# Optimization experiments

Measured on AMD Instinct MI355X. Metric: run time of the kernel, lower is better.

Reference implementation:

```python
import jax, jax.numpy as jnp
import numpy as np

L, B, S, D = 8, 1, 4096, 2048
H, KVH, HD = 16, 2, 128
Q = 32
THETA = 1e6
MROPE = (16, 24, 24)  # mrope_section, sums to HD//2
EPS = 1e-6


def setup_inputs() -> dict:
    key = jax.random.key(0)
    ks = jax.random.split(key, 8)
    hidden_states = jax.random.normal(ks[0], (L, B, S, D), dtype=jnp.float32)
    ln_w = jax.random.uniform(ks[1], (L, D), dtype=jnp.float32, minval=0.5, maxval=1.5)
    q_w = jax.random.normal(ks[2], (L, D, H * HD), dtype=jnp.float32) * 0.02
    q_b = jax.random.normal(ks[3], (L, H * HD), dtype=jnp.float32) * 0.02
    k_w = jax.random.normal(ks[4], (L, D, KVH * HD), dtype=jnp.float32) * 0.02
    k_b = jax.random.normal(ks[5], (L, KVH * HD), dtype=jnp.float32) * 0.02
    position_ids = jax.random.randint(ks[6], (3, B, S), 0, S, dtype=jnp.int32)
    q_idx = jnp.sort(jax.random.randint(ks[7], (Q,), 0, S, dtype=jnp.int32))
    return {"hidden_states": hidden_states, "ln_w": ln_w, "q_w": q_w, "q_b": q_b,
            "k_w": k_w, "k_b": k_b, "position_ids": position_ids, "q_idx": q_idx}


def _rot_half(x):
    h = x.shape[-1] // 2
    return jnp.concatenate([-x[..., h:], x[..., :h]], axis=-1)


def _mrope_combine(t):
    # t: (3, B, S, HD). Split last dim per 2*mrope_section, chunk i taken from axis i%3.
    parts, off = [], 0
    for i, sec in enumerate(MROPE):
        w = 2 * sec
        parts.append(t[i % 3, :, :, off:off + w])
        off += w
    return jnp.concatenate(parts, axis=-1)[:, None, :, :]  # (B, 1, S, HD)


def reference(hidden_states, ln_w, q_w, q_b, k_w, k_b, position_ids, q_idx):
    # Rotary embeddings from 3D mRoPE position ids
    inv_freq = 1.0 / (THETA ** (jnp.arange(0, HD, 2, dtype=jnp.float32) / HD))  # (HD/2,)
    freqs = position_ids.astype(jnp.float32)[..., None] * inv_freq  # (3, B, S, HD/2)
    emb = jnp.concatenate([freqs, freqs], axis=-1)  # (3, B, S, HD)
    cos = _mrope_combine(jnp.cos(emb))  # (B, 1, S, HD)
    sin = _mrope_combine(jnp.sin(emb))
    cos_q = cos[:, :, q_idx, :]  # (B, 1, Q, HD)
    sin_q = sin[:, :, q_idx, :]
    # Eager causal mask sliced at query rows: (Q, S)
    mask_add = jnp.where(jnp.arange(S)[None, :] > q_idx[:, None], -1e9, 0.0).astype(jnp.float32)

    scale = 1.0 / np.sqrt(HD).astype(np.float32)

    def per_layer(hs, lw, qw, qb, kw, kb):
        # RMSNorm (input_layernorm)
        var = jnp.mean(jnp.square(hs), axis=-1, keepdims=True)
        x = hs * jax.lax.rsqrt(var + EPS) * lw  # (B, S, D)
        xq = x[:, q_idx, :]  # (B, Q, D)
        k = (jnp.einsum('bsd,de->bse', x, kw) + kb).reshape(B, S, KVH, HD).transpose(0, 2, 1, 3)
        q = (jnp.einsum('bqd,de->bqe', xq, qw) + qb).reshape(B, Q, H, HD).transpose(0, 2, 1, 3)
        k = jnp.repeat(k, H // KVH, axis=1)  # repeat_kv -> (B, H, S, HD)
        k = k * cos + _rot_half(k) * sin
        q = q * cos_q + _rot_half(q) * sin_q
        scores = jnp.einsum('bhqd,bhkd->bhqk', q, k) * scale  # (B, H, Q, S)
        scores = scores + mask_add[None, None]
        return jax.nn.softmax(scores.astype(jnp.float32), axis=-1)

    return jax.vmap(per_layer)(hidden_states, ln_w, q_w, q_b, k_w, k_b)  # (L, B, H, Q, S)
```

## Files before the change

### kernel.cpp

```cpp
#include <hip/hip_runtime.h>
#include <hip/hip_bf16.h>
#include <math.h>

#define LYR 8
#define SEQ 4096
#define DIM 2048
#define NH 16
#define HD 128
#define NQ 32
#define NKV 256
#define NQE 2048

typedef __attribute__((ext_vector_type(8))) short short8;
typedef __attribute__((ext_vector_type(4))) float f32x4;

#define WS_IRQ   0
#define WS_ABLOB 256
#define WS_COS   524544
#define WS_SIN   1048832
#define WS_QBUF  1573120
#define WS_PART  2097408
#define WS_W2    4194560
#define WS_KBLOB 8388864
#define WS_QBLOB 16777472

__device__ __forceinline__ short f2bf(float x) {
  __hip_bfloat16 h = __float2bfloat16(x);
  return *(short*)&h;
}
__device__ __forceinline__ float bf2f(short s) {
  unsigned u = ((unsigned)(unsigned short)s) << 16;
  return __uint_as_float(u);
}

#define GLOAD16(srcp, dstp) \
  __builtin_amdgcn_global_load_lds( \
      (const __attribute__((address_space(1))) unsigned int*)(srcp), \
      (__attribute__((address_space(3))) unsigned int*)(dstp), 16, 0, 0)

#define RBAR() asm volatile("s_waitcnt lgkmcnt(0)\n\ts_barrier" ::: "memory")

__global__ __launch_bounds__(256) void prep_kernel(
    const float* __restrict__ ln_w, const float* __restrict__ k_w,
    short* __restrict__ W2) {
  int kb = blockIdx.x, l = blockIdx.y, t = threadIdx.x;
  const float* kwl = k_w + (size_t)l * DIM * NKV;
  const float* lnl = ln_w + l * DIM;
  short* blob = W2 + (size_t)(l * 64 + kb) * 16384;
  #pragma unroll
  for (int i = 0; i < 4; ++i) {
    int p = t + i * 256;
    int fi = p >> 6, lane = p & 63;
    int n = fi * 16 + (lane & 15);
    int k0 = kb * 32 + (lane >> 4) * 8;
    short hi8[8], lo8[8];
    #pragma unroll
    for (int e = 0; e < 8; ++e) {
      float v = lnl[k0 + e] * kwl[(size_t)(k0 + e) * NKV + n];
      short h = f2bf(v);
      hi8[e] = h;
      lo8[e] = f2bf(v - bf2f(h));
    }
    *(short8*)(blob + p * 8) = *(short8*)hi8;
    *(short8*)(blob + 8192 + p * 8) = *(short8*)lo8;
  }
}

__global__ __launch_bounds__(256) void rmsq_kernel(const float* __restrict__ hs,
                                                   const int* __restrict__ q_idx,
                                                   float* __restrict__ irq) {
  int qi = blockIdx.x, l = blockIdx.y, t = threadIdx.x;
  int s = q_idx[qi];
  const float* row = hs + ((size_t)l * SEQ + s) * DIM;
  float4 v0 = *(const float4*)(row + t * 4);
  float4 v1 = *(const float4*)(row + t * 4 + 1024);
  float acc = v0.x*v0.x + v0.y*v0.y + v0.z*v0.z + v0.w*v0.w
            + v1.x*v1.x + v1.y*v1.y + v1.z*v1.z + v1.w*v1.w;
  #pragma unroll
  for (int off = 32; off >= 1; off >>= 1) acc += __shfl_down(acc, off);
  __shared__ float red[4];
  if ((t & 63) == 0) red[t >> 6] = acc;
  __syncthreads();
  if (t == 0) {
    float tot = red[0] + red[1] + red[2] + red[3];
    irq[l * NQ + qi] = rsqrtf(tot / (float)DIM + 1e-6f);
  }
}

__global__ void cossin_kernel(const int* __restrict__ pos_ids,
                              float* __restrict__ cost, float* __restrict__ sint) {
  int idx = blockIdx.x * 256 + threadIdx.x;
  int s = idx >> 7, d = idx & 127;
  int t = (d < 32) ? 0 : (d < 80 ? 1 : 2);
  int j = d & 63;
  double invf = pow(1000000.0, -(double)j / 64.0);
  double ph = (double)pos_ids[t * SEQ + s] * invf;
  cost[idx] = (float)cos(ph);
  sint[idx] = (float)sin(ph);
}

__global__ __launch_bounds__(256) void xqt_kernel(
    const float* __restrict__ hs, const float* __restrict__ ln_w,
    const int* __restrict__ q_idx, const float* __restrict__ irq,
    short* __restrict__ Ablob) {
  __shared__ int qix[32];
  __shared__ float qir[32];
  int l = blockIdx.x, t = threadIdx.x;
  if (t < 32) { qix[t] = q_idx[t]; qir[t] = irq[l * NQ + t]; }
  __syncthreads();
  int lane = t & 63, g4 = t >> 6;
  short* base = Ablob + (size_t)l * 131072;
  int row = lane & 15, kgl = lane >> 4;
  for (int i = 0; i < 64; ++i) {
    int group = g4 * 64 + i;
    int kb = group >> 2, half = (group >> 1) & 1, mf = group & 1;
    int r = row + mf * 16;
    int k0 = kb * 32 + kgl * 8;
    const float* src = hs + ((size_t)l * SEQ + qix[r]) * DIM + k0;
    const float* lnp = ln_w + l * DIM + k0;
    float ir = qir[r];
    float4 v0 = *(const float4*)src;
    float4 v1 = *(const float4*)(src + 4);
    float4 w0 = *(const float4*)lnp;
    float4 w1 = *(const float4*)(lnp + 4);
    float av[8] = {v0.x*w0.x, v0.y*w0.y, v0.z*w0.z, v0.w*w0.w,
                   v1.x*w1.x, v1.y*w1.y, v1.z*w1.z, v1.w*w1.w};
    short o8[8];
    #pragma unroll
    for (int e = 0; e < 8; ++e) {
      float v = av[e] * ir;
      short h = f2bf(v);
      o8[e] = half ? f2bf(v - bf2f(h)) : h;
    }
    *(short8*)(base + group * 512 + lane * 8) = *(short8*)o8;
  }
}

__global__ __launch_bounds__(256) void kgemm_kernel(
    const float* __restrict__ hs, const short* __restrict__ W2,
    const float* __restrict__ k_b, const float* __restrict__ cost,
    const float* __restrict__ sint, short* __restrict__ Kblob) {
  __shared__ __align__(1024) char SM[67072];

  int t = threadIdx.x;
  int fid = blockIdx.x;
  int l = fid & 7, sb = fid >> 3;
  int s0 = sb * 64;
  int lane = t & 63, w = t >> 6;
  int fr = lane & 15, kg = lane >> 4;
  int arow = t >> 2, akg = t & 3;

  const float* hrow = hs + ((size_t)l * SEQ + s0 + arow) * DIM + akg * 8;
  const char* wbase = (const char*)(W2 + (size_t)l * 64 * 16384);
  const char* wfrag = wbase + w * 1024 + lane * 16;

  int amf = arow >> 4;
  int awoff = amf * 1024 + (((akg * 16 + (arow & 15)) * 16) ^ (akg << 5));
  int aroff = (lane * 16) ^ ((lane >> 4) << 5);

  f32x4 acc[4][4];
  #pragma unroll
  for (int mf = 0; mf < 4; ++mf)
    #pragma unroll
    for (int nf = 0; nf < 4; ++nf) acc[mf][nf] = (f32x4){0.f, 0.f, 0.f, 0.f};
  float sq = 0.f;
  float4 rA0, rA1, rB0, rB1;
  short8 B0h[4], B0l[4], B1h[4], B1l[4];

  {
    #pragma unroll
    for (int nf = 0; nf < 4; ++nf) {
      B0h[nf] = *(const short8*)(wfrag + nf * 4096);
      B0l[nf] = *(const short8*)(wfrag + nf * 4096 + 16384);
    }
    float4 a0 = *(const float4*)(hrow);
    float4 a1 = *(const float4*)(hrow + 4);
    float av[8] = {a0.x, a0.y, a0.z, a0.w, a1.x, a1.y, a1.z, a1.w};
    short hi8[8], lo8[8];
    #pragma unroll
    for (int e = 0; e < 8; ++e) {
      sq += av[e] * av[e];
      short h = f2bf(av[e]);
      hi8[e] = h;
      lo8[e] = f2bf(av[e] - bf2f(h));
    }
    *(short8*)(SM + awoff) = *(short8*)hi8;
    *(short8*)(SM + 4096 + awoff) = *(short8*)lo8;
    rA0 = *(const float4*)(hrow + 32);
    rA1 = *(const float4*)(hrow + 36);
  }
  RBAR();

#define KSTEP(KB, CA0, CA1, NA0, NA1, UBH, UBL, PBH, PBL) do { \
    int buf_ = (KB) & 1; \
    char* asb_ = SM + buf_ * 8192; \
    if ((KB) < 63) { \
      const char* bsrc_ = wfrag + (size_t)((KB) + 1) * 32768; \
      _Pragma("unroll") \
      for (int nf = 0; nf < 4; ++nf) { \
        PBH[nf] = *(const short8*)(bsrc_ + nf * 4096); \
        PBL[nf] = *(const short8*)(bsrc_ + nf * 4096 + 16384); \
      } \
    } \
    if ((KB) < 62) { \
      NA0 = *(const float4*)(hrow + ((KB) + 2) * 32); \
      NA1 = *(const float4*)(hrow + ((KB) + 2) * 32 + 4); \
    } \
    short8 ah_[4], al_[4]; \
    _Pragma("unroll") \
    for (int mf = 0; mf < 4; ++mf) { \
      ah_[mf] = *(const short8*)(asb_ + mf * 1024 + aroff); \
      al_[mf] = *(const short8*)(asb_ + 4096 + mf * 1024 + aroff); \
    } \
    __builtin_amdgcn_s_setprio(1); \
    _Pragma("unroll") \
    for (int nf = 0; nf < 4; ++nf) { \
      _Pragma("unroll") \
      for (int mf = 0; mf < 4; ++mf) { \
        acc[mf][nf] = __builtin_amdgcn_mfma_f32_16x16x32_bf16(ah_[mf], UBH[nf], acc[mf][nf], 0, 0, 0); \
        acc[mf][nf] = __builtin_amdgcn_mfma_f32_16x16x32_bf16(ah_[mf], UBL[nf], acc[mf][nf], 0, 0, 0); \
        acc[mf][nf] = __builtin_amdgcn_mfma_f32_16x16x32_bf16(al_[mf], UBH[nf], acc[mf][nf], 0, 0, 0); \
      } \
    } \
    __builtin_amdgcn_s_setprio(0); \
    if ((KB) < 63) { \
      char* asn_ = SM + (buf_ ^ 1) * 8192; \
      float av_[8] = {CA0.x, CA0.y, CA0.z, CA0.w, CA1.x, CA1.y, CA1.z, CA1.w}; \
      short hi8_[8], lo8_[8]; \
      _Pragma("unroll") \
      for (int e = 0; e < 8; ++e) { \
        sq += av_[e] * av_[e]; \
        short h_ = f2bf(av_[e]); \
        hi8_[e] = h_; \
        lo8_[e] = f2bf(av_[e] - bf2f(h_)); \
      } \
      *(short8*)(asn_ + awoff) = *(short8*)hi8_; \
      *(short8*)(asn_ + 4096 + awoff) = *(short8*)lo8_; \
    } \
    RBAR(); \
  } while (0)

  for (int kb2 = 0; kb2 < 32; ++kb2) {
    KSTEP(2 * kb2,     rA0, rA1, rB0, rB1, B0h, B0l, B1h, B1l);
    KSTEP(2 * kb2 + 1, rB0, rB1, rA0, rA1, B1h, B1l, B0h, B0l);
  }
#undef KSTEP

  sq += __shfl_xor(sq, 1);
  sq += __shfl_xor(sq, 2);
  float* irs = (float*)(SM + 66560);
  if ((t & 3) == 0) irs[arow] = rsqrtf(sq / (float)DIM + 1e-6f);
  __syncthreads();

  float* Kraw = (float*)SM;
  int j = w * 16 + fr;
  float bias0 = k_b[l * NKV + j];
  float bias1 = k_b[l * NKV + j + 64];
  float bias2 = k_b[l * NKV + j + 128];
  float bias3 = k_b[l * NKV + j + 192];
  #pragma unroll
  for (int mf = 0; mf < 4; ++mf) {
    #pragma unroll
    for (int r = 0; r < 4; ++r) {
      int row = mf * 16 + kg * 4 + r;
      int s = s0 + row;
      float ir = irs[row];
      float v0 = acc[mf][0][r] * ir + bias0;
      float v1 = acc[mf][1][r] * ir + bias1;
      float v2 = acc[mf][2][r] * ir + bias2;
      float v3 = acc[mf][3][r] * ir + bias3;
      float cj = cost[s * HD + j], sj = sint[s * HD + j];
      float cj2 = cost[s * HD + j + 64], sj2 = sint[s * HD + j + 64];
      float* kr = Kraw + row * 260;
      kr[j]       = v0 * cj - v1 * sj;
      kr[j + 64]  = v1 * cj2 + v0 * sj2;
      kr[j + 128] = v2 * cj - v3 * sj;
      kr[j + 192] = v3 * cj2 + v2 * sj2;
    }
  }
  __syncthreads();

  int kc = sb >> 1, fb = (sb & 1) * 4;
  #pragma unroll
  for (int i = 0; i < 8; ++i) {
    int c = t + i * 256;
    int lc = c & 63, fl = (c >> 6) & 3, ts = (c >> 8) & 3, kv = c >> 10;
    int key = fl * 16 + (lc & 15);
    int d0 = kv * 128 + ts * 32 + (lc >> 4) * 8;
    float4 x0 = *(const float4*)(Kraw + key * 260 + d0);
    float4 x1 = *(const float4*)(Kraw + key * 260 + d0 + 4);
    float av[8] = {x0.x, x0.y, x0.z, x0.w, x1.x, x1.y, x1.z, x1.w};
    short hi8[8], lo8[8];
    #pragma unroll
    for (int e = 0; e < 8; ++e) {
      short h = f2bf(av[e]);
      hi8[e] = h;
      lo8[e] = f2bf(av[e] - bf2f(h));
    }
    short* bb = Kblob + (size_t)((l * 2 + kv) * 32 + kc) * 32768
              + (size_t)((ts * 2 + 0) * 8 + fb + fl) * 512 + lc * 8;
    *(short8*)bb = *(short8*)hi8;
    *(short8*)(bb + 4096) = *(short8*)lo8;
  }
}

__global__ __launch_bounds__(512) void qgemm_kernel(
    const float* __restrict__ q_w, const short* __restrict__ Ablob,
    float* __restrict__ part) {
  __shared__ __align__(1024) char SM[131072];
  int t = threadIdx.x;
  int nc = blockIdx.x, ks = blockIdx.y, l = blockIdx.z;
  int lane = t & 63, w = t >> 6;
  int fr = lane & 15, kg = lane >> 4;
  const char* abase = (const char*)(Ablob + (size_t)l * 131072 + (size_t)ks * 32768);
  const float* qwl = q_w + (size_t)l * DIM * NQE;

  #pragma unroll
  for (int c = 0; c < 8; ++c) {
    int chunk = w * 8 + c;
    GLOAD16(abase + chunk * 1024 + lane * 16, SM + chunk * 1024);
  }
  #pragma unroll
  for (int c = 0; c < 4; ++c) {
    int r = w * 4 + c;
    GLOAD16((const char*)(qwl + (size_t)(ks * 512 + r) * NQE + nc * 256) + lane * 16,
            SM + 65536 + r * 1024 + lane * 16);
  }
  f32x4 acc[2][2];
  #pragma unroll
  for (int mf = 0; mf < 2; ++mf)
    #pragma unroll
    for (int nf = 0; nf < 2; ++nf) acc[mf][nf] = (f32x4){0.f, 0.f, 0.f, 0.f};
  __syncthreads();

  for (int ts = 0; ts < 16; ++ts) {
    int buf = ts & 1;
    if (ts < 15) {
      #pragma unroll
      for (int c = 0; c < 4; ++c) {
        int r = w * 4 + c;
        GLOAD16((const char*)(qwl + (size_t)(ks * 512 + (ts + 1) * 32 + r) * NQE + nc * 256) + lane * 16,
                SM + 65536 + (buf ^ 1) * 32768 + r * 1024 + lane * 16);
      }
    }
    short8 ah[2], al[2];
    #pragma unroll
    for (int mf = 0; mf < 2; ++mf) {
      ah[mf] = *(const short8*)(SM + ts * 4096 + mf * 1024 + lane * 16);
      al[mf] = *(const short8*)(SM + ts * 4096 + 2048 + mf * 1024 + lane * 16);
    }
    const float* bt = (const float*)(SM + 65536 + buf * 32768);
    #pragma unroll
    for (int nf = 0; nf < 2; ++nf) {
      int c = w * 32 + nf * 16 + fr;
      short bh8[8], bl8[8];
      #pragma unroll
      for (int e = 0; e < 8; ++e) {
        float v = bt[(kg * 8 + e) * 256 + c];
        short h = f2bf(v);
        bh8[e] = h;
        bl8[e] = f2bf(v - bf2f(h));
      }
      short8 bh = *(short8*)bh8, bl = *(short8*)bl8;
      #pragma unroll
      for (int mf = 0; mf < 2; ++mf) {
        acc[mf][nf] = __builtin_amdgcn_mfma_f32_16x16x32_bf16(ah[mf], bh, acc[mf][nf], 0, 0, 0);
        acc[mf][nf] = __builtin_amdgcn_mfma_f32_16x16x32_bf16(ah[mf], bl, acc[mf][nf], 0, 0, 0);
        acc[mf][nf] = __builtin_amdgcn_mfma_f32_16x16x32_bf16(al[mf], bh, acc[mf][nf], 0, 0, 0);
      }
    }
    __syncthreads();
  }

  #pragma unroll
  for (int mf = 0; mf < 2; ++mf) {
    #pragma unroll
    for (int r = 0; r < 4; ++r) {
      int row = mf * 16 + kg * 4 + r;
      float* prow = part + ((size_t)((ks * LYR + l) * NQ + row)) * NQE + nc * 256;
      #pragma unroll
      for (int nf = 0; nf < 2; ++nf) {
        int col = w * 32 + nf * 16 + fr;
        prow[col] = acc[mf][nf][r];
      }
    }
  }
}

__global__ __launch_bounds__(256) void qred_kernel(
    const float* __restrict__ part, const float* __restrict__ q_b,
    float* __restrict__ Qbuf) {
  int idx = blockIdx.x * 256 + threadIdx.x;
  int n = idx & 2047, q = (idx >> 11) & 31, l = idx >> 16;
  float v = q_b[l * NQE + n];
  #pragma unroll
  for (int ks = 0; ks < 4; ++ks)
    v += part[((size_t)((ks * LYR + l) * NQ + q)) * NQE + n];
  Qbuf[((size_t)l * NQ + q) * NQE + n] = v;
}

__global__ __launch_bounds__(256) void qpack_kernel(
    const float* __restrict__ Qbuf, const float* __restrict__ cost,
    const float* __restrict__ sint, const int* __restrict__ q_idx,
    short* __restrict__ Qblob) {
  int kv = blockIdx.x, l = blockIdx.y, t = threadIdx.x;
  short* blob = Qblob + (size_t)(l * 2 + kv) * 65536;
  #pragma unroll
  for (int i = 0; i < 16; ++i) {
    int p = t + i * 256;
    int ts = p >> 10, f = (p >> 6) & 15, lane = p & 63;
    int row = f * 16 + (lane & 15);
    int hh = row >> 5, q = row & 31;
    int h = kv * 8 + hh;
    int d0 = ts * 32 + (lane >> 4) * 8;
    int s = q_idx[q];
    const float* qrow = Qbuf + ((size_t)l * NQ + q) * NQE + h * HD;
    const float* ct = cost + s * HD;
    const float* st = sint + s * HD;
    short hi8[8], lo8[8];
    #pragma unroll
    for (int e = 0; e < 8; ++e) {
      int d = d0 + e;
      float x = qrow[d];
      float xp = qrow[d ^ 64];
      float v = (d < 64) ? (x * ct[d] - xp * st[d]) : (x * ct[d] + xp * st[d]);
      short h2 = f2bf(v);
      hi8[e] = h2;
      lo8[e] = f2bf(v - bf2f(h2));
    }
    *(short8*)(blob + ((ts * 2 + 0) * 16 + f) * 512 + lane * 8) = *(short8*)hi8;
    *(short8*)(blob + ((ts * 2 + 1) * 16 + f) * 512 + lane * 8) = *(short8*)lo8;
  }
}

__global__ __launch_bounds__(512) void scores_kernel(
    const short* __restrict__ Qblob, const short* __restrict__ Kblob,
    const int* __restrict__ q_idx, float* __restrict__ out) {
  __shared__ short Qs[2][16384];
  __shared__ short Ks[2][8192];
  __shared__ int qiv[32];
  int t = threadIdx.x;
  int kc = blockIdx.x, kv = blockIdx.y, l = blockIdx.z;
  int lane = t & 63, w = t >> 6;
  int wm = w >> 1, wn = w & 1;
  if (t < 32) qiv[t] = q_idx[t];
  const char* qsrc = (const char*)(Qblob + (size_t)(l * 2 + kv) * 65536);
  const char* ksrc = (const char*)(Kblob + (size_t)((l * 2 + kv) * 32 + kc) * 32768);
  #pragma unroll
  for (int c = 0; c < 4; ++c) {
    int off = (w * 4 + c) * 1024;
    GLOAD16(qsrc + off + lane * 16, (char*)Qs[0] + off);
  }
  #pragma unroll
  for (int c = 0; c < 2; ++c) {
    int off = (w * 2 + c) * 1024;
    GLOAD16(ksrc + off + lane * 16, (char*)Ks[0] + off);
  }
  f32x4 acc[4][4];
  #pragma unroll
  for (int mf = 0; mf < 4; ++mf)
    #pragma unroll
    for (int nf = 0; nf < 4; ++nf) acc[mf][nf] = (f32x4){0.f, 0.f, 0.f, 0.f};
  __syncthreads();
  for (int ts = 0; ts < 4; ++ts) {
    int buf = ts & 1;
    if (ts < 3) {
      const char* qs = qsrc + (ts + 1) * 32768;
      const char* ks = ksrc + (ts + 1) * 16384;
      #pragma unroll
      for (int c = 0; c < 4; ++c) {
        int off = (w * 4 + c) * 1024;
        GLOAD16(qs + off + lane * 16, (char*)Qs[(ts + 1) & 1] + off);
      }
      #pragma unroll
      for (int c = 0; c < 2; ++c) {
        int off = (w * 2 + c) * 1024;
        GLOAD16(ks + off + lane * 16, (char*)Ks[(ts + 1) & 1] + off);
      }
    }
    short8 ah[4], al[4];
    #pragma unroll
    for (int mf = 0; mf < 4; ++mf) {
      int f = wm * 4 + mf;
      ah[mf] = *(const short8*)(Qs[buf] + f * 512 + lane * 8);
      al[mf] = *(const short8*)(Qs[buf] + 8192 + f * 512 + lane * 8);
    }
    #pragma unroll
    for (int nf = 0; nf < 4; ++nf) {
      int f = wn * 4 + nf;
      short8 bh = *(const short8*)(Ks[buf] + f * 512 + lane * 8);
      short8 bl = *(const short8*)(Ks[buf] + 4096 + f * 512 + lane * 8);
      #pragma unroll
      for (int mf = 0; mf < 4; ++mf) {
        acc[mf][nf] = __builtin_amdgcn_mfma_f32_16x16x32_bf16(ah[mf], bh, acc[mf][nf], 0, 0, 0);
        acc[mf][nf] = __builtin_amdgcn_mfma_f32_16x16x32_bf16(ah[mf], bl, acc[mf][nf], 0, 0, 0);
        acc[mf][nf] = __builtin_amdgcn_mfma_f32_16x16x32_bf16(al[mf], bh, acc[mf][nf], 0, 0, 0);
      }
    }
    __syncthreads();
  }
  const float scale = 0.088388347648318447f;
  #pragma unroll
  for (int mf = 0; mf < 4; ++mf) {
    #pragma unroll
    for (int r = 0; r < 4; ++r) {
      int rr = wm * 64 + mf * 16 + (lane >> 4) * 4 + r;
      int hh = rr >> 5, q = rr & 31;
      int qv = qiv[q];
      float* orow = out + (((size_t)(l * NH + kv * 8 + hh)) * NQ + q) * SEQ;
      #pragma unroll
      for (int nf = 0; nf < 4; ++nf) {
        int key = kc * 128 + (wn * 4 + nf) * 16 + (lane & 15);
        orow[key] = (key > qv) ? -1e9f : acc[mf][nf][r] * scale;
      }
    }
  }
}

__global__ __launch_bounds__(256) void softmax_kernel(float* __restrict__ out) {
  size_t row = blockIdx.x;
  float* p = out + row * SEQ;
  int t = threadIdx.x;
  float4 v[4];
  float mx = -1e30f;
  #pragma unroll
  for (int i = 0; i < 4; ++i) {
    v[i] = *(const float4*)(p + t * 4 + i * 1024);
    mx = fmaxf(mx, fmaxf(fmaxf(v[i].x, v[i].y), fmaxf(v[i].z, v[i].w)));
  }
  #pragma unroll
  for (int off = 32; off >= 1; off >>= 1) mx = fmaxf(mx, __shfl_xor(mx, off));
  __shared__ float red[4];
  if ((t & 63) == 0) red[t >> 6] = mx;
  __syncthreads();
  mx = fmaxf(fmaxf(red[0], red[1]), fmaxf(red[2], red[3]));
  __syncthreads();
  float sum = 0.f;
  #pragma unroll
  for (int i = 0; i < 4; ++i) {
    v[i].x = __expf(v[i].x - mx); v[i].y = __expf(v[i].y - mx);
    v[i].z = __expf(v[i].z - mx); v[i].w = __expf(v[i].w - mx);
    sum += v[i].x + v[i].y + v[i].z + v[i].w;
  }
  #pragma unroll
  for (int off = 32; off >= 1; off >>= 1) sum += __shfl_xor(sum, off);
  if ((t & 63) == 0) red[t >> 6] = sum;
  __syncthreads();
  sum = red[0] + red[1] + red[2] + red[3];
  float inv = 1.f / sum;
  #pragma unroll
  for (int i = 0; i < 4; ++i) {
    v[i].x *= inv; v[i].y *= inv; v[i].z *= inv; v[i].w *= inv;
    *(float4*)(p + t * 4 + i * 1024) = v[i];
  }
}

extern "C" void kernel_launch(void* const* d_in, const int* in_sizes, int n_in,
                              void* d_out, int out_size, void* d_ws, size_t ws_size,
                              hipStream_t stream) {
  const float* hs   = (const float*)d_in[0];
  const float* ln_w = (const float*)d_in[1];
  const float* q_w  = (const float*)d_in[2];
  const float* q_b  = (const float*)d_in[3];
  const float* k_w  = (const float*)d_in[4];
  const float* k_b  = (const float*)d_in[5];
  const int* pos    = (const int*)d_in[6];
  const int* qidx   = (const int*)d_in[7];
  float* out = (float*)d_out;
  float* ws = (float*)d_ws;
  float* irq   = ws + WS_IRQ;
  short* Ablob = (short*)(ws + WS_ABLOB);
  float* cost  = ws + WS_COS;
  float* sint  = ws + WS_SIN;
  float* Qbuf  = ws + WS_QBUF;
  float* part  = ws + WS_PART;
  short* W2    = (short*)(ws + WS_W2);
  short* Kblob = (short*)(ws + WS_KBLOB);
  short* Qblob = (short*)(ws + WS_QBLOB);

  prep_kernel<<<dim3(64, LYR), 256, 0, stream>>>(ln_w, k_w, W2);
  rmsq_kernel<<<dim3(NQ, LYR), 256, 0, stream>>>(hs, qidx, irq);
  cossin_kernel<<<(SEQ * HD) / 256, 256, 0, stream>>>(pos, cost, sint);
  xqt_kernel<<<LYR, 256, 0, stream>>>(hs, ln_w, qidx, irq, Ablob);
  kgemm_kernel<<<512, 256, 0, stream>>>(hs, W2, k_b, cost, sint, Kblob);
  qgemm_kernel<<<dim3(8, 4, LYR), 512, 0, stream>>>(q_w, Ablob, part);
  qred_kernel<<<2048, 256, 0, stream>>>(part, q_b, Qbuf);
  qpack_kernel<<<dim3(2, LYR), 256, 0, stream>>>(Qbuf, cost, sint, qidx, Qblob);
  scores_kernel<<<dim3(32, 2, LYR), 512, 0, stream>>>(Qblob, Kblob, qidx, out);
  softmax_kernel<<<LYR * NH * NQ, 256, 0, stream>>>(out);
}
```

Before: 279.8 us.

## Stage four K-steps of A per LDS buffer to cut barriers in K GEMM

The K-projection GEMM now converts and stores 128 columns (four K-steps) of hidden states into each LDS double-buffer half, instead of 32 columns. That means one barrier per four K-steps rather than one per step, and global A loads are issued a whole chunk ahead. B fragments are still register double-buffered per sub-step. The cost is a larger LDS footprint (64KB A staging) and more live registers for the eight prefetched float4s, which may hurt occupancy or register pressure.

```diff
diff --git a/kernel.cpp b/kernel.cpp
--- a/kernel.cpp
+++ b/kernel.cpp
@@ -140,7 +140,7 @@
     const float* __restrict__ hs, const short* __restrict__ W2,
     const float* __restrict__ k_b, const float* __restrict__ cost,
     const float* __restrict__ sint, short* __restrict__ Kblob) {
-  __shared__ __align__(1024) char SM[67072];
+  __shared__ __align__(1024) char SM[66816];
 
   int t = threadIdx.x;
   int fid = blockIdx.x;
@@ -154,8 +154,7 @@
   const char* wbase = (const char*)(W2 + (size_t)l * 64 * 16384);
   const char* wfrag = wbase + w * 1024 + lane * 16;
 
-  int amf = arow >> 4;
-  int awoff = amf * 1024 + (((akg * 16 + (arow & 15)) * 16) ^ (akg << 5));
+  int awoff = (arow >> 4) * 1024 + (((akg * 16 + (arow & 15)) * 16) ^ (akg << 5));
   int aroff = (lane * 16) ^ ((lane >> 4) << 5);
 
   f32x4 acc[4][4];
@@ -164,17 +163,12 @@
     #pragma unroll
     for (int nf = 0; nf < 4; ++nf) acc[mf][nf] = (f32x4){0.f, 0.f, 0.f, 0.f};
   float sq = 0.f;
-  float4 rA0, rA1, rB0, rB1;
   short8 B0h[4], B0l[4], B1h[4], B1l[4];
 
-  {
-    #pragma unroll
-    for (int nf = 0; nf < 4; ++nf) {
-      B0h[nf] = *(const short8*)(wfrag + nf * 4096);
-      B0l[nf] = *(const short8*)(wfrag + nf * 4096 + 16384);
-    }
-    float4 a0 = *(const float4*)(hrow);
-    float4 a1 = *(const float4*)(hrow + 4);
+  #pragma unroll
+  for (int s = 0; s < 4; ++s) {
+    float4 a0 = *(const float4*)(hrow + s * 32);
+    float4 a1 = *(const float4*)(hrow + s * 32 + 4);
     float av[8] = {a0.x, a0.y, a0.z, a0.w, a1.x, a1.y, a1.z, a1.w};
     short hi8[8], lo8[8];
     #pragma unroll
@@ -184,67 +178,99 @@
       hi8[e] = h;
       lo8[e] = f2bf(av[e] - bf2f(h));
     }
-    *(short8*)(SM + awoff) = *(short8*)hi8;
-    *(short8*)(SM + 4096 + awoff) = *(short8*)lo8;
-    rA0 = *(const float4*)(hrow + 32);
-    rA1 = *(const float4*)(hrow + 36);
+    *(short8*)(SM + s * 8192 + awoff) = *(short8*)hi8;
+    *(short8*)(SM + s * 8192 + 4096 + awoff) = *(short8*)lo8;
+  }
+  #pragma unroll
+  for (int nf = 0; nf < 4; ++nf) {
+    B0h[nf] = *(const short8*)(wfrag + nf * 4096);
+    B0l[nf] = *(const short8*)(wfrag + nf * 4096 + 16384);
   }
   RBAR();
 
-#define KSTEP(KB, CA0, CA1, NA0, NA1, UBH, UBL, PBH, PBL) do { \
-    int buf_ = (KB) & 1; \
-    char* asb_ = SM + buf_ * 8192; \
-    if ((KB) < 63) { \
-      const char* bsrc_ = wfrag + (size_t)((KB) + 1) * 32768; \
-      _Pragma("unroll") \
-      for (int nf = 0; nf < 4; ++nf) { \
-        PBH[nf] = *(const short8*)(bsrc_ + nf * 4096); \
-        PBL[nf] = *(const short8*)(bsrc_ + nf * 4096 + 16384); \
-      } \
-    } \
-    if ((KB) < 62) { \
-      NA0 = *(const float4*)(hrow + ((KB) + 2) * 32); \
-      NA1 = *(const float4*)(hrow + ((KB) + 2) * 32 + 4); \
-    } \
-    short8 ah_[4], al_[4]; \
-    _Pragma("unroll") \
-    for (int mf = 0; mf < 4; ++mf) { \
-      ah_[mf] = *(const short8*)(asb_ + mf * 1024 + aroff); \
-      al_[mf] = *(const short8*)(asb_ + 4096 + mf * 1024 + aroff); \
-    } \
-    __builtin_amdgcn_s_setprio(1); \
-    _Pragma("unroll") \
-    for (int nf = 0; nf < 4; ++nf) { \
-      _Pragma("unroll") \
-      for (int mf = 0; mf < 4; ++mf) { \
-        acc[mf][nf] = __builtin_amdgcn_mfma_f32_16x16x32_bf16(ah_[mf], UBH[nf], acc[mf][nf], 0, 0, 0); \
-        acc[mf][nf] = __builtin_amdgcn_mfma_f32_16x16x32_bf16(ah_[mf], UBL[nf], acc[mf][nf], 0, 0, 0); \
-        acc[mf][nf] = __builtin_amdgcn_mfma_f32_16x16x32_bf16(al_[mf], UBH[nf], acc[mf][nf], 0, 0, 0); \
-      } \
-    } \
-    __builtin_amdgcn_s_setprio(0); \
-    if ((KB) < 63) { \
-      char* asn_ = SM + (buf_ ^ 1) * 8192; \
-      float av_[8] = {CA0.x, CA0.y, CA0.z, CA0.w, CA1.x, CA1.y, CA1.z, CA1.w}; \
-      short hi8_[8], lo8_[8]; \
-      _Pragma("unroll") \
-      for (int e = 0; e < 8; ++e) { \
-        sq += av_[e] * av_[e]; \
-        short h_ = f2bf(av_[e]); \
-        hi8_[e] = h_; \
-        lo8_[e] = f2bf(av_[e] - bf2f(h_)); \
-      } \
-      *(short8*)(asn_ + awoff) = *(short8*)hi8_; \
-      *(short8*)(asn_ + 4096 + awoff) = *(short8*)lo8_; \
-    } \
-    RBAR(); \
-  } while (0)
-
-  for (int kb2 = 0; kb2 < 32; ++kb2) {
-    KSTEP(2 * kb2,     rA0, rA1, rB0, rB1, B0h, B0l, B1h, B1l);
-    KSTEP(2 * kb2 + 1, rB0, rB1, rA0, rA1, B1h, B1l, B0h, B0l);
-  }
-#undef KSTEP
+  for (int ch = 0; ch < 16; ++ch) {
+    int buf = ch & 1;
+    const char* abuf = SM + buf * 32768;
+    char* anext = SM + (buf ^ 1) * 32768;
+
+    float4 cA[8];
+    if (ch < 15) {
+      #pragma unroll
+      for (int s = 0; s < 4; ++s) {
+        cA[s * 2]     = *(const float4*)(hrow + (ch + 1) * 128 + s * 32);
+        cA[s * 2 + 1] = *(const float4*)(hrow + (ch + 1) * 128 + s * 32 + 4);
+      }
+    }
+
+    #pragma unroll
+    for (int s = 0; s < 4; ++s) {
+      if (s < 3 || ch < 15) {
+        const char* bsrc = wfrag + (size_t)(ch * 4 + s + 1) * 32768;
+        if ((s & 1) == 0) {
+          #pragma unroll
+          for (int nf = 0; nf < 4; ++nf) {
+            B1h[nf] = *(const short8*)(bsrc + nf * 4096);
+            B1l[nf] = *(const short8*)(bsrc + nf * 4096 + 16384);
+          }
+        } else {
+          #pragma unroll
+          for (int nf = 0; nf < 4; ++nf) {
+            B0h[nf] = *(const short8*)(bsrc + nf * 4096);
+            B0l[nf] = *(const short8*)(bsrc + nf * 4096 + 16384);
+          }
+        }
+      }
+      short8 ah[4], al[4];
+      #pragma unroll
+      for (int mf = 0; mf < 4; ++mf) {
+        ah[mf] = *(const short8*)(abuf + s * 8192 + mf * 1024 + aroff);
+        al[mf] = *(const short8*)(abuf + s * 8192 + 4096 + mf * 1024 + aroff);
+      }
+      __builtin_amdgcn_s_setprio(1);
+      if ((s & 1) == 0) {
+        #pragma unroll
+        for (int nf = 0; nf < 4; ++nf) {
+          #pragma unroll
+          for (int mf = 0; mf < 4; ++mf) {
+            acc[mf][nf] = __builtin_amdgcn_mfma_f32_16x16x32_bf16(ah[mf], B0h[nf], acc[mf][nf], 0, 0, 0);
+            acc[mf][nf] = __builtin_amdgcn_mfma_f32_16x16x32_bf16(ah[mf], B0l[nf], acc[mf][nf], 0, 0, 0);
+            acc[mf][nf] = __builtin_amdgcn_mfma_f32_16x16x32_bf16(al[mf], B0h[nf], acc[mf][nf], 0, 0, 0);
+          }
+        }
+      } else {
+        #pragma unroll
+        for (int nf = 0; nf < 4; ++nf) {
+          #pragma unroll
+          for (int mf = 0; mf < 4; ++mf) {
+            acc[mf][nf] = __builtin_amdgcn_mfma_f32_16x16x32_bf16(ah[mf], B1h[nf], acc[mf][nf], 0, 0, 0);
+            acc[mf][nf] = __builtin_amdgcn_mfma_f32_16x16x32_bf16(ah[mf], B1l[nf], acc[mf][nf], 0, 0, 0);
+            acc[mf][nf] = __builtin_amdgcn_mfma_f32_16x16x32_bf16(al[mf], B1h[nf], acc[mf][nf], 0, 0, 0);
+          }
+        }
+      }
+      __builtin_amdgcn_s_setprio(0);
+    }
+
+    if (ch < 15) {
+      #pragma unroll
+      for (int s = 0; s < 4; ++s) {
+        float4 a0 = cA[s * 2];
+        float4 a1 = cA[s * 2 + 1];
+        float av[8] = {a0.x, a0.y, a0.z, a0.w, a1.x, a1.y, a1.z, a1.w};
+        short hi8[8], lo8[8];
+        #pragma unroll
+        for (int e = 0; e < 8; ++e) {
+          sq += av[e] * av[e];
+          short h = f2bf(av[e]);
+          hi8[e] = h;
+          lo8[e] = f2bf(av[e] - bf2f(h));
+        }
+        *(short8*)(anext + s * 8192 + awoff) = *(short8*)hi8;
+        *(short8*)(anext + s * 8192 + 4096 + awoff) = *(short8*)lo8;
+      }
+    }
+    RBAR();
+  }
 
   sq += __shfl_xor(sq, 1);
   sq += __shfl_xor(sq, 2);
```

Result: no change. 276.8 us (-1.1%).
